# Optimization experiments

Hardware: AMD Instinct MI355X
Metric: run time of the kernel (lower is better)

## Reference

```python
import jax, jax.numpy as jnp
import numpy as np
import math

B, S, D_MODEL = 2, 2048, 1024
H = 16
DK = D_MODEL // H          # 64, down-proj per-stream dim
NOPE, ROPE = 128, 64
D_HEAD = NOPE + ROPE       # 192 = d_latent // H
D_LATENT = H * D_HEAD      # 3072
ROT_DIM = 2 * ((ROPE // 2) // 2)  # rotary dim actually rotated = qk_rope_dim//2 = 32
EPS = 1e-6


def _rmsnorm(x, w):
    out = x * jax.lax.rsqrt(jnp.mean(x * x, axis=-1, keepdims=True) + EPS)
    return out * w


def _apply_rope(x):
    # x: [b, h, s, d]; rotate first ROT_DIM channels, interleaved pairing
    s = x.shape[-2]
    inv_freq = 1.0 / (10000.0 ** (jnp.arange(0, ROT_DIM, 2, dtype=jnp.float32) / ROT_DIM))
    freqs = jnp.arange(s, dtype=jnp.float32)[:, None] * inv_freq[None, :]  # [s, ROT_DIM//2]
    freqs = jnp.repeat(freqs, 2, axis=-1)  # [s, ROT_DIM], (f0,f0,f1,f1,...)
    cos, sin = jnp.cos(freqs), jnp.sin(freqs)
    xl, xr = x[..., :ROT_DIM], x[..., ROT_DIM:]
    x1, x2 = xl[..., 0::2], xl[..., 1::2]
    rot = jnp.stack([-x2, x1], axis=-1).reshape(xl.shape)
    xl = xl * cos + rot * sin
    return jnp.concatenate([xl, xr], axis=-1)


def setup_inputs() -> dict:
    key = jax.random.key(0)
    ks = jax.random.split(key, 5)
    sc = 0.02
    x = jax.random.normal(ks[0], (B, S, D_MODEL), jnp.float32)
    mask = jnp.broadcast_to(jnp.tril(jnp.ones((S, S), jnp.int32)), (B, S, S))
    w_down = jax.random.normal(ks[1], (D_MODEL, 3 * DK), jnp.float32) * sc
    rms_w = jnp.ones((3 * DK,), jnp.float32)
    w_up = jax.random.normal(ks[2], (3 * DK, 3 * D_LATENT), jnp.float32) * sc
    w_o = jax.random.normal(ks[3], (D_LATENT, D_MODEL), jnp.float32) * sc
    return {"x": x, "mask": mask, "w_down": w_down, "rms_w": rms_w, "w_up": w_up, "w_o": w_o}


def reference(x, mask, w_down, rms_w, w_up, w_o):
    h = x @ w_down                        # [b, s, 3*dk]
    h = _rmsnorm(h, rms_w)
    qkv = h @ w_up                        # [b, s, 3*d_latent]
    q, k, v = jnp.split(qkv, 3, axis=-1)  # each [b, s, d_latent]

    def to_heads(t):
        # einops '(d h)': d outer, h inner
        return t.reshape(B, S, D_HEAD, H).transpose(0, 3, 1, 2)  # [b, h, s, d]

    q, k, v = to_heads(q), to_heads(k), to_heads(v)
    q_nope, q_rope = q[..., :NOPE], q[..., NOPE:]
    k_nope, k_rope = k[..., :NOPE], k[..., NOPE:]
    q_rope = _apply_rope(q_rope)
    k_rope = _apply_rope(k_rope)

    scores = (jnp.einsum('bhid,bhjd->bhij', q_nope, k_nope)
              + jnp.einsum('bhid,bhjd->bhij', q_rope, k_rope))
    scores = scores / math.sqrt(NOPE + ROPE)
    scores = jnp.where(mask[:, None] == 0, -1e9, scores)
    attn = jax.nn.softmax(scores, axis=-1)

    out = jnp.einsum('bhij,bhjd->bhid', attn, v)        # [b, h, s, d]
    out = out.transpose(0, 2, 1, 3).reshape(B, S, D_LATENT)  # 'b h s d -> b s (h d)'
    return out @ w_o
```

## Files before the change

### kernel.cpp

```cpp
#include <hip/hip_runtime.h>
#include <stdint.h>
#include <stddef.h>


typedef __bf16 bf16x8 __attribute__((ext_vector_type(8)));
typedef float  f32x4  __attribute__((ext_vector_type(4)));

#define MFMA16x16(a,b,c) __builtin_amdgcn_mfma_f32_16x16x32_bf16((a),(b),(c),0,0,0)

__device__ __forceinline__ uint16_t f2bf(float f){
  union { float f; uint32_t u; } v; v.f = f;
  uint32_t u = v.u + 0x7fffu + ((v.u >> 16) & 1u);
  return (uint16_t)(u >> 16);
}
__device__ __forceinline__ bf16x8 load_frag(const uint16_t* p){
  uint4 u = *reinterpret_cast<const uint4*>(p);
  return __builtin_bit_cast(bf16x8, u);
}
__device__ __forceinline__ f32x4 fzero(){
  f32x4 z = {0.f, 0.f, 0.f, 0.f};
  return z;
}
__device__ __forceinline__ uint32_t pack2(float a, float b){
  return (uint32_t)f2bf(a) | ((uint32_t)f2bf(b) << 16);
}
__device__ __forceinline__ void gl2lds16(const uint16_t* g, uint16_t* l){
  __builtin_amdgcn_global_load_lds(
      (const __attribute__((address_space(1))) uint32_t*)g,
      (__attribute__((address_space(3))) uint32_t*)l,
      16, 0, 0);
}

__global__ __launch_bounds__(256) void k_transpose_cvt(const float* __restrict__ in,
                                                       uint16_t* __restrict__ out,
                                                       int R, int C){
  __shared__ float t[32][33];
  const int tc = blockIdx.x * 32;
  const int tr = blockIdx.y * 32;
  const int j = threadIdx.x & 31, i0 = threadIdx.x >> 5;
  for(int ii = 0; ii < 4; ++ii){
    int r = i0 + ii * 8;
    t[r][j] = in[(size_t)(tr + r) * C + tc + j];
  }
  __syncthreads();
  for(int ii = 0; ii < 4; ++ii){
    int c = i0 + ii * 8;
    out[(size_t)(tc + c) * R + tr + j] = f2bf(t[j][c]);
  }
}

__global__ __launch_bounds__(256) void k_down_mfma(const float* __restrict__ x,
                                                   const uint16_t* __restrict__ wdt,
                                                   const float* __restrict__ rms_w,
                                                   uint16_t* __restrict__ h_out){
  __shared__ __align__(16) uint16_t as[32 * 64];
  __shared__ float hsq[32];
  const int tid  = threadIdx.x;
  const int wave = tid >> 6, lane = tid & 63;
  const int ml = lane & 15, qd = lane >> 4;
  const int m0 = blockIdx.x * 32;
  const int n0w = wave * 48;
  if(tid < 32) hsq[tid] = 0.f;

  f32x4 acc[2][3];
#pragma unroll
  for(int mt = 0; mt < 2; ++mt)
#pragma unroll
    for(int nt = 0; nt < 3; ++nt) acc[mt][nt] = fzero();

  const int srow = tid >> 3, sc = tid & 7;
  for(int kt = 0; kt < 16; ++kt){
    const float* src = x + (size_t)(m0 + srow) * 1024 + kt * 64 + sc * 8;
    float4 a = *reinterpret_cast<const float4*>(src);
    float4 b = *reinterpret_cast<const float4*>(src + 4);
    uint4 pk;
    pk.x = pack2(a.x, a.y); pk.y = pack2(a.z, a.w);
    pk.z = pack2(b.x, b.y); pk.w = pack2(b.z, b.w);
    __syncthreads();
    *reinterpret_cast<uint4*>(as + srow * 64 + ((sc ^ (srow & 7)) * 8)) = pk;
    __syncthreads();
#pragma unroll
    for(int kk = 0; kk < 2; ++kk){
      bf16x8 af[2];
#pragma unroll
      for(int mt = 0; mt < 2; ++mt){
        int row = mt * 16 + ml;
        af[mt] = load_frag(as + row * 64 + (((kk * 4 + qd) ^ (row & 7)) * 8));
      }
#pragma unroll
      for(int nt = 0; nt < 3; ++nt){
        bf16x8 bfr = load_frag(wdt + (size_t)(n0w + nt * 16 + ml) * 1024 + kt * 64 + kk * 32 + qd * 8);
#pragma unroll
        for(int mt = 0; mt < 2; ++mt)
          acc[mt][nt] = MFMA16x16(af[mt], bfr, acc[mt][nt]);
      }
    }
  }
  __syncthreads();
#pragma unroll
  for(int mt = 0; mt < 2; ++mt)
#pragma unroll
    for(int r = 0; r < 4; ++r){
      float s = acc[mt][0][r]*acc[mt][0][r] + acc[mt][1][r]*acc[mt][1][r] + acc[mt][2][r]*acc[mt][2][r];
#pragma unroll
      for(int off = 1; off < 16; off <<= 1) s += __shfl_xor(s, off);
      if(ml == 0) atomicAdd(&hsq[mt * 16 + qd * 4 + r], s);
    }
  __syncthreads();
  float rw[3];
#pragma unroll
  for(int nt = 0; nt < 3; ++nt) rw[nt] = rms_w[n0w + nt * 16 + ml];
#pragma unroll
  for(int mt = 0; mt < 2; ++mt)
#pragma unroll
    for(int r = 0; r < 4; ++r){
      int row = mt * 16 + qd * 4 + r;
      float scl = rsqrtf(hsq[row] * (1.0f / 192.0f) + 1e-6f);
#pragma unroll
      for(int nt = 0; nt < 3; ++nt)
        h_out[(size_t)(m0 + row) * 192 + n0w + nt * 16 + ml] = f2bf(acc[mt][nt][r] * scl * rw[nt]);
    }
}

__global__ __launch_bounds__(256) void k_gemm_up(const uint16_t* __restrict__ hmat,
                                                 const uint16_t* __restrict__ wt,
                                                 uint16_t* __restrict__ q_t,
                                                 uint16_t* __restrict__ k_t,
                                                 uint16_t* __restrict__ v_t){
  __shared__ __align__(16) uint16_t rp[16 * 129 * 8];
  const int wave = threadIdx.x >> 6, lane = threadIdx.x & 63;
  const int ml = lane & 15, qd = lane >> 4;
  const int m0 = blockIdx.y * 32;
  const int bx = blockIdx.x;
  const int which = bx / 6;
  const int d0b = (bx % 6) * 32;
  const int n0w = bx * 512 + wave * 128;
  const int d0w = d0b + wave * 8;

  bf16x8 af[2][6];
#pragma unroll
  for(int mt = 0; mt < 2; ++mt)
#pragma unroll
    for(int kk = 0; kk < 6; ++kk)
      af[mt][kk] = load_frag(hmat + (size_t)(m0 + mt * 16 + ml) * 192 + kk * 32 + qd * 8);

  f32x4 acc[8][2];
#pragma unroll
  for(int nt = 0; nt < 8; ++nt){ acc[nt][0] = fzero(); acc[nt][1] = fzero(); }
#pragma unroll
  for(int nt = 0; nt < 8; ++nt){
#pragma unroll
    for(int kk = 0; kk < 6; ++kk){
      bf16x8 b = load_frag(wt + (size_t)(n0w + nt * 16 + ml) * 192 + kk * 32 + qd * 8);
      acc[nt][0] = MFMA16x16(af[0][kk], b, acc[nt][0]);
      acc[nt][1] = MFMA16x16(af[1][kk], b, acc[nt][1]);
    }
  }

  const int b   = m0 >> 11;
  const int s0  = m0 & 2047;
  const int kt2 = s0 >> 6;
  const int row0 = s0 & 63;
  uint4* rp4 = (uint4*)rp;

  if(which < 2){
    const float qs = which ? 1.0f : 0.07216878364870322f;
    const bool rope = (d0w >= 128) && (d0w < 160);
#pragma unroll
    for(int mt = 0; mt < 2; ++mt)
#pragma unroll
      for(int r = 0; r < 4; ++r){
        int t = mt * 16 + qd * 4 + r;
        int s = s0 + t;
        float v[8];
#pragma unroll
        for(int nt = 0; nt < 8; ++nt) v[nt] = acc[nt][mt][r] * qs;
        if(rope){
#pragma unroll
          for(int pi = 0; pi < 4; ++pi){
            int fi = (d0w + 2 * pi - 128) >> 1;
            float invf = __expf(-(float)fi * 0.5756462732485114f);
            float sn, cs;
            sincosf((float)s * invf, &sn, &cs);
            float e = v[2 * pi], o = v[2 * pi + 1];
            v[2 * pi]     = e * cs - o * sn;
            v[2 * pi + 1] = o * cs + e * sn;
          }
        }
        uint4 pk;
        pk.x = pack2(v[0], v[1]); pk.y = pack2(v[2], v[3]);
        pk.z = pack2(v[4], v[5]); pk.w = pack2(v[6], v[7]);
        rp4[ml * 129 + t * 4 + (wave ^ (t & 3))] = pk;
      }
  } else {
#pragma unroll
    for(int nt = 0; nt < 8; ++nt){
      int dl = wave * 8 + nt;
#pragma unroll
      for(int mt = 0; mt < 2; ++mt){
        int jc = mt * 2 + (qd >> 1);
        int slot = ml * 129 + dl * 4 + (jc ^ (dl & 3));
        uint2 pk;
        pk.x = pack2(acc[nt][mt][0], acc[nt][mt][1]);
        pk.y = pack2(acc[nt][mt][2], acc[nt][mt][3]);
        *(reinterpret_cast<uint2*>(rp + slot * 8) + (qd & 1)) = pk;
      }
    }
  }
  __syncthreads();

  if(which < 2){
    uint16_t* dst = which ? k_t : q_t;
    const int cb = d0b >> 3;
#pragma unroll
    for(int it = 0; it < 8; ++it){
      int h = wave * 4 + (it & 3), rhalf = it >> 2;
      int tloc = rhalf * 16 + (lane >> 2), p = lane & 3;
      int row = row0 + tloc;
      uint4 val = rp4[h * 129 + tloc * 4 + p];
      size_t off = ((size_t)(b * 16 + h) * 32 + kt2) * 12288
                 + (size_t)row * 192 + ((cb ^ (tloc & 4)) + p) * 8;
      *reinterpret_cast<uint4*>(dst + off) = val;
    }
  } else {
    const int cs0 = row0 >> 3;
#pragma unroll
    for(int it = 0; it < 8; ++it){
      int h = wave * 4 + (it & 3), dhalf = it >> 2;
      int dl = dhalf * 16 + (lane >> 2), p = lane & 3;
      uint4 val = rp4[h * 129 + dl * 4 + p];
      size_t off = ((size_t)(b * 16 + h) * 32 + kt2) * 12288
                 + (size_t)(d0b + dl) * 64 + ((cs0 ^ (dl & 4)) + p) * 8;
      *reinterpret_cast<uint4*>(v_t + off) = val;
    }
  }
}

__global__ __launch_bounds__(512, 2) void k_attn(const uint16_t* __restrict__ q_t,
                                                 const uint16_t* __restrict__ k_t,
                                                 const uint16_t* __restrict__ v_t,
                                                 uint16_t* __restrict__ attn_out){
  __shared__ __align__(16) uint16_t kb[2][64 * 192];
  __shared__ __align__(16) uint16_t vb[2][208 * 64];
  __shared__ __align__(16) uint16_t psw_all[8][16 * 64];
  const int tid  = threadIdx.x;
  const int wave = tid >> 6;
  const int lane = tid & 63;
  const int ml   = lane & 15;
  const int qd   = lane >> 4;
  const int bh   = blockIdx.x & 31;
  const int pr   = blockIdx.x >> 5;

  {
    uint32_t* v0 = (uint32_t*)(vb[0] + 192 * 64);
    uint32_t* v1 = (uint32_t*)(vb[1] + 192 * 64);
    v0[tid] = 0x3F803F80u;
    v1[tid] = 0x3F803F80u;
  }

  const uint16_t* kbase = k_t + (size_t)bh * 32 * 12288;
  const uint16_t* vbase = v_t + (size_t)bh * 32 * 12288;
  const uint16_t* qbase = q_t + (size_t)bh * 32 * 12288;
  const int hh = bh & 15, bb = bh >> 4;

  auto qblock = [&](int qb){
    const int last = 2 * qb + 1;
    {
#pragma unroll
      for(int it = 0; it < 3; ++it){
        int seg = it * 8 + wave;
        gl2lds16(kbase + seg * 512 + lane * 8, kb[0] + seg * 512);
      }
#pragma unroll
      for(int it = 0; it < 3; ++it){
        int seg = it * 8 + wave;
        gl2lds16(vbase + seg * 512 + lane * 8, vb[0] + seg * 512);
      }
      const uint16_t* qt0 = qbase + (size_t)qb * 2 * 12288;
#pragma unroll
      for(int it = 0; it < 6; ++it){
        int seg = it * 8 + wave;
        uint16_t* dst = (seg < 24) ? (kb[1] + seg * 512) : (vb[1] + (seg - 24) * 512);
        gl2lds16(qt0 + seg * 512 + lane * 8, dst);
      }
    }
    __builtin_amdgcn_sched_barrier(0);
    asm volatile("s_waitcnt vmcnt(0) lgkmcnt(0)" ::: "memory");
    __builtin_amdgcn_sched_barrier(0);
    __builtin_amdgcn_s_barrier();

    bf16x8 qf[6];
    {
      int row = wave * 16 + ml;
      const uint16_t* qsrc = (row < 64) ? (kb[1] + row * 192)
                                        : (vb[1] + (row - 64) * 192);
#pragma unroll
      for(int kk = 0; kk < 6; ++kk)
        qf[kk] = load_frag(qsrc + (((kk * 4 + qd) ^ (row & 7)) * 8));
    }
    asm volatile("s_waitcnt lgkmcnt(0)" ::: "memory");
    __builtin_amdgcn_sched_barrier(0);
    __builtin_amdgcn_s_barrier();

    f32x4 o[13];
#pragma unroll
    for(int i = 0; i < 13; ++i) o[i] = fzero();

    const int r0 = qb * 128 + wave * 16;
    int cur = 0;
    for(int kt = 0; kt <= last; ++kt){
      if(kt < last){
        const uint16_t* kn = kbase + (size_t)(kt + 1) * 12288;
        const uint16_t* vn = vbase + (size_t)(kt + 1) * 12288;
#pragma unroll
        for(int it = 0; it < 3; ++it){
          int seg = it * 8 + wave;
          gl2lds16(kn + seg * 512 + lane * 8, kb[cur ^ 1] + seg * 512);
        }
#pragma unroll
        for(int it = 0; it < 3; ++it){
          int seg = it * 8 + wave;
          gl2lds16(vn + seg * 512 + lane * 8, vb[cur ^ 1] + seg * 512);
        }
        __builtin_amdgcn_sched_barrier(0);
        asm volatile("s_waitcnt vmcnt(6)" ::: "memory");
        __builtin_amdgcn_sched_barrier(0);
      } else {
        asm volatile("s_waitcnt vmcnt(0)" ::: "memory");
        __builtin_amdgcn_sched_barrier(0);
      }
      __builtin_amdgcn_s_barrier();

      const int lo = kt * 64;
      if(lo <= r0 + 15){
        const bool diag = (lo + 63 > r0);
        float p[4][4];
        const uint16_t* kc = kb[cur];
        __builtin_amdgcn_s_setprio(1);
#pragma unroll
        for(int nt = 0; nt < 4; ++nt){
          f32x4 a = fzero();
          int row = nt * 16 + ml;
#pragma unroll
          for(int kk = 0; kk < 6; ++kk){
            bf16x8 b = load_frag(kc + row * 192 + (((kk * 4 + qd) ^ (row & 7)) * 8));
            a = MFMA16x16(qf[kk], b, a);
          }
#pragma unroll
          for(int r = 0; r < 4; ++r) p[nt][r] = a[r];
        }
        __builtin_amdgcn_s_setprio(0);
#pragma unroll
        for(int nt = 0; nt < 4; ++nt)
#pragma unroll
          for(int r = 0; r < 4; ++r){
            float v = p[nt][r];
            if(diag){
              int i = r0 + qd * 4 + r;
              int j = lo + nt * 16 + ml;
              if(j > i) v = -1e9f;
            }
            p[nt][r] = __expf(v);
          }
        uint16_t* psw = psw_all[wave];
#pragma unroll
        for(int nt = 0; nt < 4; ++nt)
#pragma unroll
          for(int r = 0; r < 4; ++r){
            int rp2 = qd * 4 + r;
            int col = nt * 16 + ml;
            int c = (col >> 3) ^ (rp2 & 7);
            psw[rp2 * 64 + c * 8 + (col & 7)] = f2bf(p[nt][r]);
          }
        const uint16_t* vc = vb[cur];
        __builtin_amdgcn_s_setprio(1);
#pragma unroll
        for(int kk2 = 0; kk2 < 2; ++kk2){
          int cp = (kk2 * 4 + qd) ^ (ml & 7);
          bf16x8 pa = load_frag(psw + ml * 64 + cp * 8);
#pragma unroll
          for(int dt = 0; dt < 13; ++dt){
            int row = dt * 16 + ml;
            int cv = (kk2 * 4 + qd) ^ (row & 7);
            bf16x8 vbf = load_frag(vc + row * 64 + cv * 8);
            o[dt] = MFMA16x16(pa, vbf, o[dt]);
          }
        }
        __builtin_amdgcn_s_setprio(0);
      }
      __builtin_amdgcn_s_barrier();
      cur ^= 1;
    }

#pragma unroll
    for(int r = 0; r < 4; ++r){
      int i = r0 + qd * 4 + r;
      float inv = 1.0f / o[12][r];
      size_t obase = ((size_t)bb * 2048 + i) * 3072 + hh * 192;
#pragma unroll
      for(int dt = 0; dt < 12; ++dt)
        attn_out[obase + dt * 16 + ml] = f2bf(o[dt][r] * inv);
    }
  };

  qblock(15 - pr);
  qblock(pr);
  asm volatile("s_waitcnt vmcnt(0)" ::: "memory");
}

__global__ __launch_bounds__(256) void k_gemm_o_tile(const uint16_t* __restrict__ a,
                                                     const uint16_t* __restrict__ wt,
                                                     float* __restrict__ part){
  __shared__ __align__(16) uint16_t as[128 * 64];
  __shared__ __align__(16) uint16_t bs[128 * 64];
  const int wave = threadIdx.x >> 6, lane = threadIdx.x & 63;
  const int ml = lane & 15, qd = lane >> 4;
  const int m0 = blockIdx.y * 128, n0 = blockIdx.x * 128;
  const int kz = blockIdx.z;
  const int mo = (wave >> 1) * 64, no = (wave & 1) * 64;

  const int lrow = lane >> 3;
  const int gch  = (lane & 7) ^ (lrow & 7);
  const uint16_t* abase = a  + (size_t)(m0 + lrow) * 3072 + kz * 1536 + gch * 8;
  const uint16_t* bbase = wt + (size_t)(n0 + lrow) * 3072 + kz * 1536 + gch * 8;

  f32x4 acc[4][4];
#pragma unroll
  for(int mt = 0; mt < 4; ++mt)
#pragma unroll
    for(int nt = 0; nt < 4; ++nt) acc[mt][nt] = fzero();

  for(int kt = 0; kt < 24; ++kt){
    __syncthreads();
#pragma unroll
    for(int it = 0; it < 4; ++it){
      int seg = it * 4 + wave;
      gl2lds16(abase + (size_t)seg * 24576 + kt * 64, as + seg * 512);
      gl2lds16(bbase + (size_t)seg * 24576 + kt * 64, bs + seg * 512);
    }
    __syncthreads();
#pragma unroll
    for(int ks2 = 0; ks2 < 2; ++ks2){
      bf16x8 af[4], bfr[4];
#pragma unroll
      for(int mt = 0; mt < 4; ++mt){
        int row = mo + mt * 16 + ml;
        af[mt] = load_frag(as + row * 64 + (((ks2 * 4 + qd) ^ (row & 7)) * 8));
      }
#pragma unroll
      for(int nt = 0; nt < 4; ++nt){
        int row = no + nt * 16 + ml;
        bfr[nt] = load_frag(bs + row * 64 + (((ks2 * 4 + qd) ^ (row & 7)) * 8));
      }
#pragma unroll
      for(int mt = 0; mt < 4; ++mt)
#pragma unroll
        for(int nt = 0; nt < 4; ++nt)
          acc[mt][nt] = MFMA16x16(af[mt], bfr[nt], acc[mt][nt]);
    }
  }

  float* dst = part + (size_t)kz * 4096 * 1024;
#pragma unroll
  for(int mt = 0; mt < 4; ++mt)
#pragma unroll
    for(int nt = 0; nt < 4; ++nt)
#pragma unroll
      for(int r = 0; r < 4; ++r){
        int row = m0 + mo + mt * 16 + qd * 4 + r;
        int col = n0 + no + nt * 16 + ml;
        dst[(size_t)row * 1024 + col] = acc[mt][nt][r];
      }
}

__global__ __launch_bounds__(256) void k_addout(const float* __restrict__ part,
                                                float* __restrict__ out){
  int i = blockIdx.x * 256 + threadIdx.x;
  const float4* p0 = (const float4*)part;
  const float4* p1 = p0 + (size_t)1048576;
  float4 a = p0[i], b = p1[i];
  float4 c; c.x = a.x + b.x; c.y = a.y + b.y; c.z = a.z + b.z; c.w = a.w + b.w;
  ((float4*)out)[i] = c;
}


extern "C" void kernel_launch(void* const* d_in, const int* in_sizes, int n_in,
                              void* d_out, int out_size, void* d_ws, size_t ws_size,
                              hipStream_t stream) {
  (void)in_sizes; (void)n_in; (void)out_size; (void)ws_size;
  const float* x      = (const float*)d_in[0];
  const float* w_down = (const float*)d_in[2];
  const float* rms_w  = (const float*)d_in[3];
  const float* w_up   = (const float*)d_in[4];
  const float* w_o    = (const float*)d_in[5];
  float* out = (float*)d_out;

  char* ws = (char*)d_ws;
  uint16_t* h_bf   = (uint16_t*)(ws);
  uint16_t* w_up_t = (uint16_t*)(ws + 1572864);
  uint16_t* w_o_t  = (uint16_t*)(ws + 5111808);
  uint16_t* w_dn_t = (uint16_t*)(ws + 11403264);
  uint16_t* q_tb   = (uint16_t*)(ws + 11796480);
  uint16_t* k_tb   = (uint16_t*)(ws + 36962304);
  uint16_t* v_tb   = (uint16_t*)(ws + 62128128);
  uint16_t* attnO  = (uint16_t*)(ws + 87293952);
  float*    part   = (float*)(ws + 11796480);

  k_transpose_cvt<<<dim3(288, 6), 256, 0, stream>>>(w_up, w_up_t, 192, 9216);
  k_transpose_cvt<<<dim3(32, 96), 256, 0, stream>>>(w_o,  w_o_t,  3072, 1024);
  k_transpose_cvt<<<dim3(6, 32),  256, 0, stream>>>(w_down, w_dn_t, 1024, 192);
  k_down_mfma<<<128, 256, 0, stream>>>(x, w_dn_t, rms_w, h_bf);
  k_gemm_up<<<dim3(18, 128), 256, 0, stream>>>(h_bf, w_up_t, q_tb, k_tb, v_tb);
  k_attn<<<256, 512, 0, stream>>>(q_tb, k_tb, v_tb, attnO);
  k_gemm_o_tile<<<dim3(8, 32, 2), 256, 0, stream>>>(attnO, w_o_t, part);
  k_addout<<<4096, 256, 0, stream>>>(part, out);
}
```

Measured before the change: 337.5 us.

## Restructure attention: one q-block per block, 32-key tiles, smaller LDS for 4 blocks/CU

The attention kernel now gives each workgroup a single 128-row query block instead of a balanced pair, and launches twice as many blocks. Key tiles shrink from 64 to 32 rows. K and V staging are split across wave halves, with V gathered from the existing 64-row layout through precomputed swizzled offsets. Shared memory is cut to about 60 KB and launch bounds are raised to 4 blocks per CU to improve occupancy and latency hiding. In exchange there are more barriers per key, loop iterations do less work each, and load balance now depends on block scheduling instead of explicit pairing.

```diff
diff --git a/kernel.cpp b/kernel.cpp
--- a/kernel.cpp
+++ b/kernel.cpp
@@ -236,176 +236,177 @@
   }
 }
 
-__global__ __launch_bounds__(512, 2) void k_attn(const uint16_t* __restrict__ q_t,
+__global__ __launch_bounds__(512, 4) void k_attn(const uint16_t* __restrict__ q_t,
                                                  const uint16_t* __restrict__ k_t,
                                                  const uint16_t* __restrict__ v_t,
                                                  uint16_t* __restrict__ attn_out){
-  __shared__ __align__(16) uint16_t kb[2][64 * 192];
-  __shared__ __align__(16) uint16_t vb[2][208 * 64];
-  __shared__ __align__(16) uint16_t psw_all[8][16 * 64];
+  __shared__ __align__(16) uint16_t smem[30720];
   const int tid  = threadIdx.x;
   const int wave = tid >> 6;
   const int lane = tid & 63;
   const int ml   = lane & 15;
   const int qd   = lane >> 4;
-  const int bh   = blockIdx.x & 31;
-  const int pr   = blockIdx.x >> 5;
-
+  const int B    = blockIdx.x;
+  const int bh   = B & 31;
+  const int prr  = B >> 5;
+  const int qb   = (prr < 8) ? (15 - prr) : (prr - 8);
+  const int last = 4 * qb + 3;
+
+  uint16_t* const kbuf0 = smem;
+  uint16_t* const kbuf1 = smem + 6144;
+  uint16_t* const vbuf0 = smem + 12288;
+  uint16_t* const vbuf1 = smem + 18944;
+  uint16_t* const psw   = smem + 25600 + wave * 640;
+
+  const uint16_t* kbase = k_t + (size_t)bh * 393216;
+  const uint16_t* vbase = v_t + (size_t)bh * 393216;
+  const uint16_t* qbase = q_t + (size_t)bh * 393216 + (size_t)qb * 24576;
+  const int hh = bh & 15, bb = bh >> 4;
+
+  int voffE[3], voffO[3];
   {
-    uint32_t* v0 = (uint32_t*)(vb[0] + 192 * 64);
-    uint32_t* v1 = (uint32_t*)(vb[1] + 192 * 64);
-    v0[tid] = 0x3F803F80u;
-    v1[tid] = 0x3F803F80u;
-  }
-
-  const uint16_t* kbase = k_t + (size_t)bh * 32 * 12288;
-  const uint16_t* vbase = v_t + (size_t)bh * 32 * 12288;
-  const uint16_t* qbase = q_t + (size_t)bh * 32 * 12288;
-  const int hh = bh & 15, bb = bh >> 4;
-
-  auto qblock = [&](int qb){
-    const int last = 2 * qb + 1;
-    {
-#pragma unroll
-      for(int it = 0; it < 3; ++it){
-        int seg = it * 8 + wave;
-        gl2lds16(kbase + seg * 512 + lane * 8, kb[0] + seg * 512);
-      }
-#pragma unroll
-      for(int it = 0; it < 3; ++it){
-        int seg = it * 8 + wave;
-        gl2lds16(vbase + seg * 512 + lane * 8, vb[0] + seg * 512);
-      }
-      const uint16_t* qt0 = qbase + (size_t)qb * 2 * 12288;
-#pragma unroll
-      for(int it = 0; it < 6; ++it){
-        int seg = it * 8 + wave;
-        uint16_t* dst = (seg < 24) ? (kb[1] + seg * 512) : (vb[1] + (seg - 24) * 512);
-        gl2lds16(qt0 + seg * 512 + lane * 8, dst);
-      }
-    }
-    __builtin_amdgcn_sched_barrier(0);
-    asm volatile("s_waitcnt vmcnt(0) lgkmcnt(0)" ::: "memory");
-    __builtin_amdgcn_sched_barrier(0);
+    const int w3 = (wave & 3) * 3;
+#pragma unroll
+    for(int it = 0; it < 3; ++it){
+      int seg = w3 + it;
+      int rp_ = seg * 8 + (lane >> 3);
+      int x   = (lane & 7) ^ (rp_ & 7);
+      int d   = rp_ * 2 + (x >> 2);
+      int c   = x & 3;
+      voffE[it] = d * 64 + (((0 + c) ^ (d & 7)) * 8);
+      voffO[it] = d * 64 + (((4 + c) ^ (d & 7)) * 8);
+    }
+  }
+  const int vpoff = (ml >> 1) * 64 + ((((ml & 1) * 4 + qd) ^ (ml >> 1)) * 8);
+
+  {
+    const int s0 = wave * 6;
+#pragma unroll
+    for(int it = 0; it < 6; ++it){
+      int seg = s0 + it;
+      gl2lds16(qbase + seg * 512 + lane * 8, smem + seg * 512);
+    }
+  }
+  __builtin_amdgcn_sched_barrier(0);
+  asm volatile("s_waitcnt vmcnt(0)" ::: "memory");
+  __builtin_amdgcn_sched_barrier(0);
+  __builtin_amdgcn_s_barrier();
+
+  bf16x8 qf[6];
+  {
+    int row = wave * 16 + ml;
+#pragma unroll
+    for(int kk = 0; kk < 6; ++kk)
+      qf[kk] = load_frag(smem + row * 192 + (((kk * 4 + qd) ^ (row & 7)) * 8));
+  }
+  asm volatile("s_waitcnt lgkmcnt(0)" ::: "memory");
+  __builtin_amdgcn_sched_barrier(0);
+  __builtin_amdgcn_s_barrier();
+
+  if(tid < 256) ((uint32_t*)(vbuf0 + 6144))[tid] = 0x3F803F80u;
+  else          ((uint32_t*)(vbuf1 + 6144))[tid - 256] = 0x3F803F80u;
+
+  auto stage = [&](int t, int sel){
+    const int w3 = (wave & 3) * 3;
+    if(wave < 4){
+      const uint16_t* src = kbase + t * 6144 + w3 * 512 + lane * 8;
+      uint16_t* dst = (sel ? kbuf1 : kbuf0) + w3 * 512;
+      gl2lds16(src, dst);
+      gl2lds16(src + 512, dst + 512);
+      gl2lds16(src + 1024, dst + 1024);
+    } else {
+      const uint16_t* srcb = vbase + (size_t)(t >> 1) * 12288;
+      uint16_t* dst = (sel ? vbuf1 : vbuf0) + w3 * 512;
+      if(t & 1){
+        gl2lds16(srcb + voffO[0], dst);
+        gl2lds16(srcb + voffO[1], dst + 512);
+        gl2lds16(srcb + voffO[2], dst + 1024);
+      } else {
+        gl2lds16(srcb + voffE[0], dst);
+        gl2lds16(srcb + voffE[1], dst + 512);
+        gl2lds16(srcb + voffE[2], dst + 1024);
+      }
+    }
+  };
+
+  stage(0, 0);
+
+  f32x4 o[13];
+#pragma unroll
+  for(int i = 0; i < 13; ++i) o[i] = fzero();
+
+  const int r0 = qb * 128 + wave * 16;
+  int cur = 0;
+  for(int kt = 0; kt <= last; ++kt){
+    if(kt < last){
+      stage(kt + 1, cur ^ 1);
+      __builtin_amdgcn_sched_barrier(0);
+      asm volatile("s_waitcnt vmcnt(3)" ::: "memory");
+      __builtin_amdgcn_sched_barrier(0);
+    } else {
+      asm volatile("s_waitcnt vmcnt(0)" ::: "memory");
+      __builtin_amdgcn_sched_barrier(0);
+    }
     __builtin_amdgcn_s_barrier();
 
-    bf16x8 qf[6];
-    {
-      int row = wave * 16 + ml;
-      const uint16_t* qsrc = (row < 64) ? (kb[1] + row * 192)
-                                        : (vb[1] + (row - 64) * 192);
-#pragma unroll
-      for(int kk = 0; kk < 6; ++kk)
-        qf[kk] = load_frag(qsrc + (((kk * 4 + qd) ^ (row & 7)) * 8));
-    }
-    asm volatile("s_waitcnt lgkmcnt(0)" ::: "memory");
-    __builtin_amdgcn_sched_barrier(0);
+    if(kt * 32 <= r0 + 15){
+      const uint16_t* kc = cur ? kbuf1 : kbuf0;
+      const uint16_t* vc = cur ? vbuf1 : vbuf0;
+      float p[2][4];
+      __builtin_amdgcn_s_setprio(1);
+#pragma unroll
+      for(int nt = 0; nt < 2; ++nt){
+        f32x4 a = fzero();
+        int row = nt * 16 + ml;
+#pragma unroll
+        for(int kk = 0; kk < 6; ++kk){
+          bf16x8 b = load_frag(kc + row * 192 + (((kk * 4 + qd) ^ (row & 7)) * 8));
+          a = MFMA16x16(qf[kk], b, a);
+        }
+#pragma unroll
+        for(int r = 0; r < 4; ++r) p[nt][r] = a[r];
+      }
+      __builtin_amdgcn_s_setprio(0);
+      const bool diag = (kt * 32 + 31 > r0);
+#pragma unroll
+      for(int nt = 0; nt < 2; ++nt)
+#pragma unroll
+        for(int r = 0; r < 4; ++r){
+          float v = p[nt][r];
+          if(diag){
+            int i = r0 + qd * 4 + r;
+            int j = kt * 32 + nt * 16 + ml;
+            if(j > i) v = -1e9f;
+          }
+          p[nt][r] = __expf(v);
+        }
+#pragma unroll
+      for(int nt = 0; nt < 2; ++nt)
+#pragma unroll
+        for(int r = 0; r < 4; ++r)
+          psw[(qd * 4 + r) * 40 + nt * 16 + ml] = f2bf(p[nt][r]);
+      bf16x8 pa = load_frag(psw + ml * 40 + qd * 8);
+      __builtin_amdgcn_s_setprio(1);
+#pragma unroll
+      for(int dt = 0; dt < 13; ++dt){
+        bf16x8 vbf = load_frag(vc + vpoff + dt * 512);
+        o[dt] = MFMA16x16(pa, vbf, o[dt]);
+      }
+      __builtin_amdgcn_s_setprio(0);
+    }
     __builtin_amdgcn_s_barrier();
-
-    f32x4 o[13];
-#pragma unroll
-    for(int i = 0; i < 13; ++i) o[i] = fzero();
-
-    const int r0 = qb * 128 + wave * 16;
-    int cur = 0;
-    for(int kt = 0; kt <= last; ++kt){
-      if(kt < last){
-        const uint16_t* kn = kbase + (size_t)(kt + 1) * 12288;
-        const uint16_t* vn = vbase + (size_t)(kt + 1) * 12288;
-#pragma unroll
-        for(int it = 0; it < 3; ++it){
-          int seg = it * 8 + wave;
-          gl2lds16(kn + seg * 512 + lane * 8, kb[cur ^ 1] + seg * 512);
-        }
-#pragma unroll
-        for(int it = 0; it < 3; ++it){
-          int seg = it * 8 + wave;
-          gl2lds16(vn + seg * 512 + lane * 8, vb[cur ^ 1] + seg * 512);
-        }
-        __builtin_amdgcn_sched_barrier(0);
-        asm volatile("s_waitcnt vmcnt(6)" ::: "memory");
-        __builtin_amdgcn_sched_barrier(0);
-      } else {
-        asm volatile("s_waitcnt vmcnt(0)" ::: "memory");
-        __builtin_amdgcn_sched_barrier(0);
-      }
-      __builtin_amdgcn_s_barrier();
-
-      const int lo = kt * 64;
-      if(lo <= r0 + 15){
-        const bool diag = (lo + 63 > r0);
-        float p[4][4];
-        const uint16_t* kc = kb[cur];
-        __builtin_amdgcn_s_setprio(1);
-#pragma unroll
-        for(int nt = 0; nt < 4; ++nt){
-          f32x4 a = fzero();
-          int row = nt * 16 + ml;
-#pragma unroll
-          for(int kk = 0; kk < 6; ++kk){
-            bf16x8 b = load_frag(kc + row * 192 + (((kk * 4 + qd) ^ (row & 7)) * 8));
-            a = MFMA16x16(qf[kk], b, a);
-          }
-#pragma unroll
-          for(int r = 0; r < 4; ++r) p[nt][r] = a[r];
-        }
-        __builtin_amdgcn_s_setprio(0);
-#pragma unroll
-        for(int nt = 0; nt < 4; ++nt)
-#pragma unroll
-          for(int r = 0; r < 4; ++r){
-            float v = p[nt][r];
-            if(diag){
-              int i = r0 + qd * 4 + r;
-              int j = lo + nt * 16 + ml;
-              if(j > i) v = -1e9f;
-            }
-            p[nt][r] = __expf(v);
-          }
-        uint16_t* psw = psw_all[wave];
-#pragma unroll
-        for(int nt = 0; nt < 4; ++nt)
-#pragma unroll
-          for(int r = 0; r < 4; ++r){
-            int rp2 = qd * 4 + r;
-            int col = nt * 16 + ml;
-            int c = (col >> 3) ^ (rp2 & 7);
-            psw[rp2 * 64 + c * 8 + (col & 7)] = f2bf(p[nt][r]);
-          }
-        const uint16_t* vc = vb[cur];
-        __builtin_amdgcn_s_setprio(1);
-#pragma unroll
-        for(int kk2 = 0; kk2 < 2; ++kk2){
-          int cp = (kk2 * 4 + qd) ^ (ml & 7);
-          bf16x8 pa = load_frag(psw + ml * 64 + cp * 8);
-#pragma unroll
-          for(int dt = 0; dt < 13; ++dt){
-            int row = dt * 16 + ml;
-            int cv = (kk2 * 4 + qd) ^ (row & 7);
-            bf16x8 vbf = load_frag(vc + row * 64 + cv * 8);
-            o[dt] = MFMA16x16(pa, vbf, o[dt]);
-          }
-        }
-        __builtin_amdgcn_s_setprio(0);
-      }
-      __builtin_amdgcn_s_barrier();
-      cur ^= 1;
-    }
-
-#pragma unroll
-    for(int r = 0; r < 4; ++r){
-      int i = r0 + qd * 4 + r;
-      float inv = 1.0f / o[12][r];
-      size_t obase = ((size_t)bb * 2048 + i) * 3072 + hh * 192;
-#pragma unroll
-      for(int dt = 0; dt < 12; ++dt)
-        attn_out[obase + dt * 16 + ml] = f2bf(o[dt][r] * inv);
-    }
-  };
-
-  qblock(15 - pr);
-  qblock(pr);
-  asm volatile("s_waitcnt vmcnt(0)" ::: "memory");
+    cur ^= 1;
+  }
+
+#pragma unroll
+  for(int r = 0; r < 4; ++r){
+    int i = r0 + qd * 4 + r;
+    float inv = 1.0f / o[12][r];
+    size_t obase = ((size_t)bb * 2048 + i) * 3072 + hh * 192;
+#pragma unroll
+    for(int dt = 0; dt < 12; ++dt)
+      attn_out[obase + dt * 16 + ml] = f2bf(o[dt][r] * inv);
+  }
 }
 
 __global__ __launch_bounds__(256) void k_gemm_o_tile(const uint16_t* __restrict__ a,
@@ -511,7 +512,7 @@
   k_transpose_cvt<<<dim3(6, 32),  256, 0, stream>>>(w_down, w_dn_t, 1024, 192);
   k_down_mfma<<<128, 256, 0, stream>>>(x, w_dn_t, rms_w, h_bf);
   k_gemm_up<<<dim3(18, 128), 256, 0, stream>>>(h_bf, w_up_t, q_tb, k_tb, v_tb);
-  k_attn<<<256, 512, 0, stream>>>(q_tb, k_tb, v_tb, attnO);
+  k_attn<<<512, 512, 0, stream>>>(q_tb, k_tb, v_tb, attnO);
   k_gemm_o_tile<<<dim3(8, 32, 2), 256, 0, stream>>>(attnO, w_o_t, part);
   k_addout<<<4096, 256, 0, stream>>>(part, out);
 }
```

After: 348.5 us. 3.3% more time.
